# Kernel optimization log

Measured on AMD Instinct MI355X. Metric: run time of the kernel, lower is better.

## Reference

```python
import jax, jax.numpy as jnp
import numpy as np

B, N, P_FEATS = 8, 4096, 3
WIDTH, HEADS, LAYERS, N_LAT = 768, 12, 8, 256
NUM_FREQS = 8
D_HEAD = WIDTH // HEADS
SCALE = 1.0 / np.sqrt(np.sqrt(D_HEAD))  # applied to q and k separately
IN_DIM = 3 * (1 + 2 * NUM_FREQS) + P_FEATS  # 54
EPS = 1e-5


def fourier_embed(pc):
    # pc: [B,N,3] -> [B,N,51] (include_input + sin/cos at freqs 2^0..2^7)
    freqs = (2.0 ** jnp.arange(NUM_FREQS)).astype(pc.dtype)
    ang = pc[..., None] * freqs  # [B,N,3,F]
    ang = ang.reshape(*pc.shape[:-1], 3 * NUM_FREQS)
    return jnp.concatenate([pc, jnp.sin(ang), jnp.cos(ang)], axis=-1)


def layernorm(x, s, b):
    mu = jnp.mean(x, axis=-1, keepdims=True)
    var = jnp.mean(jnp.square(x - mu), axis=-1, keepdims=True)
    return (x - mu) * jax.lax.rsqrt(var + EPS) * s + b


def mh_attn(q, k, v):
    # q: [B,T,H,C], k/v: [B,S,H,C]
    w = jnp.einsum('bthc,bshc->bhts', q * SCALE, k * SCALE)
    w = jax.nn.softmax(w.astype(jnp.float32), axis=-1).astype(q.dtype)
    out = jnp.einsum('bhts,bshc->bthc', w, v)
    return out.reshape(*q.shape[:2], -1)


def setup_inputs() -> dict:
    key = jax.random.key(0)
    ks = iter(jax.random.split(key, 64))
    rn = lambda shape, std=0.02: jax.random.normal(next(ks), shape, jnp.float32) * std
    inp = {
        'pc': jax.random.normal(next(ks), (B, N, 3), jnp.float32),
        'feats': jax.random.uniform(next(ks), (B, N, P_FEATS), jnp.float32),
        'query': rn((N_LAT, WIDTH)),
        'in_W': rn((WIDTH, IN_DIM)), 'in_b': jnp.zeros((WIDTH,)),
        'ca_qkv_W': rn((3 * WIDTH, WIDTH)), 'ca_qkv_b': jnp.zeros((3 * WIDTH,)),
        'ca_proj_W': rn((WIDTH, WIDTH)), 'ca_proj_b': jnp.zeros((WIDTH,)),
        'ln1_s': jnp.ones((LAYERS, WIDTH)), 'ln1_b': jnp.zeros((LAYERS, WIDTH)),
        'qkv_W': rn((LAYERS, 3 * WIDTH, WIDTH)), 'qkv_b': jnp.zeros((LAYERS, 3 * WIDTH)),
        'proj_W': rn((LAYERS, WIDTH, WIDTH)), 'proj_b': jnp.zeros((LAYERS, WIDTH)),
        'ln2_s': jnp.ones((LAYERS, WIDTH)), 'ln2_b': jnp.zeros((LAYERS, WIDTH)),
        'fc_W': rn((LAYERS, 4 * WIDTH, WIDTH)), 'fc_b': jnp.zeros((LAYERS, 4 * WIDTH)),
        'fc2_W': rn((LAYERS, WIDTH, 4 * WIDTH)), 'fc2_b': jnp.zeros((LAYERS, WIDTH)),
    }
    return inp


def _forward(pc, feats, query, in_W, in_b, ca_qkv_W, ca_qkv_b, ca_proj_W, ca_proj_b,
             ln1_s, ln1_b, qkv_W, qkv_b, proj_W, proj_b, ln2_s, ln2_b,
             fc_W, fc_b, fc2_W, fc2_b):
    bs = pc.shape[0]
    data = jnp.concatenate([fourier_embed(pc), feats], axis=-1)  # [B,N,54]
    data = data @ in_W.T + in_b  # [B,N,W]
    q_lat = jnp.broadcast_to(query[None], (bs, N_LAT, WIDTH))

    # --- cross attention (no residual, matching source) ---
    q = (q_lat @ ca_qkv_W.T + ca_qkv_b)[..., :WIDTH]
    kv = data @ ca_qkv_W.T + ca_qkv_b
    k, v = kv[..., WIDTH:2 * WIDTH], kv[..., 2 * WIDTH:]
    q = q.reshape(bs, N_LAT, HEADS, D_HEAD)
    k = k.reshape(bs, N, HEADS, D_HEAD)
    v = v.reshape(bs, N, HEADS, D_HEAD)
    latents = mh_attn(q, k, v) @ ca_proj_W.T + ca_proj_b  # [B,L,W]

    # --- self-attention transformer stack via scan ---
    def block(x, p):
        (l1s, l1b, qW, qb, pW, pb, l2s, l2b, fW, fb, f2W, f2b) = p
        h = layernorm(x, l1s, l1b)
        qkv = (h @ qW.T + qb).reshape(bs, N_LAT, HEADS, 3 * D_HEAD)
        qh, kh, vh = jnp.split(qkv, 3, axis=-1)
        x = x + mh_attn(qh, kh, vh) @ pW.T + pb
        h = layernorm(x, l2s, l2b)
        h = jax.nn.gelu(h @ fW.T + fb, approximate=False) @ f2W.T + f2b
        return x + h, None

    params = (ln1_s, ln1_b, qkv_W, qkv_b, proj_W, proj_b, ln2_s, ln2_b, fc_W, fc_b, fc2_W, fc2_b)
    latents, _ = jax.lax.scan(block, latents, params)
    return latents, pc


def reference(pc, feats, query, in_W, in_b, ca_qkv_W, ca_qkv_b, ca_proj_W, ca_proj_b,
              ln1_s, ln1_b, qkv_W, qkv_b, proj_W, proj_b, ln2_s, ln2_b,
              fc_W, fc_b, fc2_W, fc2_b):
    return _forward(pc, feats, query, in_W, in_b, ca_qkv_W, ca_qkv_b, ca_proj_W, ca_proj_b,
                    ln1_s, ln1_b, qkv_W, qkv_b, proj_W, proj_b, ln2_s, ln2_b,
                    fc_W, fc_b, fc2_W, fc2_b)
```

## Files before the change

kernel.cpp:

```cpp
#include <hip/hip_runtime.h>
#include <stdint.h>

typedef unsigned short u16;
typedef __bf16 bf16x8 __attribute__((ext_vector_type(8)));
typedef float f32x4 __attribute__((ext_vector_type(4)));

#define DEVINL __device__ __forceinline__

DEVINL u16 f2bf(float f) {
  union { float f; unsigned u; } c; c.f = f;
  unsigned u = c.u + 0x7FFFu + ((c.u >> 16) & 1u);
  return (u16)(u >> 16);
}

DEVINL float bf2f(u16 v) {
  union { unsigned u; float f; } c; c.u = (unsigned)v << 16;
  return c.f;
}

DEVINL unsigned pk2bf(float a, float b) {
#if __has_builtin(__builtin_amdgcn_cvt_pk_bf16_f32)
  auto r = __builtin_amdgcn_cvt_pk_bf16_f32(a, b);
  unsigned u;
  __builtin_memcpy(&u, &r, 4);
  return u;
#else
  return (unsigned)f2bf(a) | ((unsigned)f2bf(b) << 16);
#endif
}

DEVINL void gl2lds16(const void* g, void* l) {
  __builtin_amdgcn_global_load_lds(
      (const __attribute__((address_space(1))) unsigned int*)g,
      (__attribute__((address_space(3))) unsigned int*)l, 16, 0, 0);
}

__global__ __launch_bounds__(256) void cvt4_kernel(
    const float* __restrict__ s0, u16* __restrict__ d0, int n0,
    const float* __restrict__ s1, u16* __restrict__ d1, int n1,
    const float* __restrict__ s2, u16* __restrict__ d2, int n2,
    const float* __restrict__ s3, u16* __restrict__ d3, int n3) {
  int i = blockIdx.x * 256 + threadIdx.x;
  const float* s; u16* d;
  if (i < n0) { s = s0; d = d0; }
  else {
    i -= n0;
    if (i < n1) { s = s1; d = d1; }
    else {
      i -= n1;
      if (i < n2) { s = s2; d = d2; }
      else {
        i -= n2;
        if (i >= n3) return;
        s = s3; d = d3;
      }
    }
  }
  float4 v = ((const float4*)s)[i];
  ((uint2*)d)[i] = make_uint2(pk2bf(v.x, v.y), pk2bf(v.z, v.w));
}

__global__ __launch_bounds__(256) void pad_inwT_kernel(const float* __restrict__ src,
                                                       u16* __restrict__ dst) {
  int t = blockIdx.x * 256 + threadIdx.x;
  if (t >= 64 * 768) return;
  int j = t / 768, o = t - j * 768;
  dst[t] = (j < 54) ? f2bf(src[o * 54 + j]) : (u16)0;
}

__global__ __launch_bounds__(256) void bprime_kernel(const float* __restrict__ caW,
                                                     const float* __restrict__ caB,
                                                     const float* __restrict__ inb,
                                                     float* __restrict__ bp) {
  int w = threadIdx.x >> 6, lane = threadIdx.x & 63;
  int m = blockIdx.x * 4 + w;
  const float* row = caW + (size_t)(768 + m) * 768;
  float s = 0.f;
#pragma unroll
  for (int k = 0; k < 12; k++) s += row[lane + k * 64] * inb[lane + k * 64];
#pragma unroll
  for (int msk = 32; msk >= 1; msk >>= 1) s += __shfl_xor(s, msk, 64);
  if (lane == 0) bp[m] = s + caB[768 + m];
}

__global__ __launch_bounds__(256) void embed_kernel(const float* __restrict__ pc,
                                                    const float* __restrict__ feats,
                                                    u16* __restrict__ emb) {
  int t = blockIdx.x * 256 + threadIdx.x;
  int p = t >> 6, c = t & 63;
  float v = 0.f;
  if (c < 3) {
    v = pc[p * 3 + c];
  } else if (c < 27) {
    int i = c - 3;
    float f = (float)(1 << (i & 7));
    v = sinf(pc[p * 3 + (i >> 3)] * f);
  } else if (c < 51) {
    int i = c - 27;
    float f = (float)(1 << (i & 7));
    v = cosf(pc[p * 3 + (i >> 3)] * f);
  } else if (c < 54) {
    v = feats[p * 3 + (c - 51)];
  }
  emb[t] = f2bf(v);
}

template <int TM, int TN, int WR, int WC, int MODE>
__global__ __launch_bounds__(256) void gemm_t(
    const u16* __restrict__ A, const u16* __restrict__ Bw,
    const float* __restrict__ bias, const float* __restrict__ resid,
    float* __restrict__ outF, u16* __restrict__ outB,
    int M, int N, int Nout, int K, int gelu,
    u16* __restrict__ vt, int vy, int skvt, int bsh) {
  constexpr int IM = TM / WR / 16;
  constexpr int IN = TN / WC / 16;
  __shared__ u16 As[TM * 32];
  __shared__ u16 Bs[TN * 32];
  const int tid = threadIdx.x;
  const int lane = tid & 63, w = tid >> 6;
  const int l15 = lane & 15, quad = lane >> 4;
  const int mblk = blockIdx.x * TM, nblk = blockIdx.y * TN;
  const int wm = (w % WR) * (TM / WR);
  const int wn = (w / WR) * (TN / WC);

  f32x4 acc[IM][IN];
#pragma unroll
  for (int i = 0; i < IM; i++)
#pragma unroll
    for (int j = 0; j < IN; j++) acc[i][j] = f32x4{0.f, 0.f, 0.f, 0.f};

  bool tv = false;
  if (MODE == 1) tv = ((int)blockIdx.y >= vy);
  if (MODE == 2) tv = ((int)(blockIdx.y % 3) == 2);

  if (!tv) {
    for (int k0 = 0; k0 < K; k0 += 32) {
#pragma unroll
      for (int s = tid; s < TM * 4; s += 256) {
        int row = s >> 2, c8 = (s & 3) << 3;
        gl2lds16(A + (size_t)(mblk + row) * K + (k0 + c8), &As[s * 8]);
      }
#pragma unroll
      for (int s = tid; s < TN * 4; s += 256) {
        int row = s >> 2, c8 = (s & 3) << 3;
        gl2lds16(Bw + (size_t)(nblk + row) * K + (k0 + c8), &Bs[s * 8]);
      }
      __syncthreads();
      bf16x8 af[IM], bfr[IN];
#pragma unroll
      for (int i = 0; i < IM; i++)
        af[i] = *(const bf16x8*)&As[(wm + i * 16 + l15) * 32 + quad * 8];
#pragma unroll
      for (int j = 0; j < IN; j++)
        bfr[j] = *(const bf16x8*)&Bs[(wn + j * 16 + l15) * 32 + quad * 8];
#pragma unroll
      for (int i = 0; i < IM; i++)
#pragma unroll
        for (int j = 0; j < IN; j++)
          acc[i][j] = __builtin_amdgcn_mfma_f32_16x16x32_bf16(bfr[j], af[i], acc[i][j], 0, 0, 0);
      __syncthreads();
    }
#pragma unroll
    for (int i = 0; i < IM; i++) {
      int m = mblk + wm + i * 16 + l15;
#pragma unroll
      for (int j = 0; j < IN; j++) {
        int n0 = nblk + wn + j * 16 + quad * 4;
        float4 bv = bias ? *(const float4*)&bias[n0] : make_float4(0.f, 0.f, 0.f, 0.f);
        float v0 = acc[i][j][0] + bv.x;
        float v1 = acc[i][j][1] + bv.y;
        float v2 = acc[i][j][2] + bv.z;
        float v3 = acc[i][j][3] + bv.w;
        if (gelu) {
          v0 = 0.5f * v0 * (1.0f + erff(v0 * 0.70710678118f));
          v1 = 0.5f * v1 * (1.0f + erff(v1 * 0.70710678118f));
          v2 = 0.5f * v2 * (1.0f + erff(v2 * 0.70710678118f));
          v3 = 0.5f * v3 * (1.0f + erff(v3 * 0.70710678118f));
        }
        size_t idx = (size_t)m * Nout + n0;
        if (resid) {
          float4 rv = *(const float4*)&resid[idx];
          v0 += rv.x; v1 += rv.y; v2 += rv.z; v3 += rv.w;
        }
        if (outF) {
          float4 ov = {v0, v1, v2, v3};
          *(float4*)&outF[idx] = ov;
        }
        if (outB) {
          *(uint2*)&outB[idx] = make_uint2(pk2bf(v0, v1), pk2bf(v2, v3));
        }
      }
    }
  } else {
    for (int k0 = 0; k0 < K; k0 += 32) {
#pragma unroll
      for (int s = tid; s < TM * 4; s += 256) {
        int row = s >> 2, c8 = (s & 3) << 3;
        gl2lds16(A + (size_t)(mblk + row) * K + (k0 + c8), &As[s * 8]);
      }
#pragma unroll
      for (int s = tid; s < TN * 4; s += 256) {
        int row = s >> 2, c8 = (s & 3) << 3;
        gl2lds16(Bw + (size_t)(nblk + row) * K + (k0 + c8), &Bs[s * 8]);
      }
      __syncthreads();
      bf16x8 af[IM], bfr[IN];
#pragma unroll
      for (int i = 0; i < IM; i++)
        af[i] = *(const bf16x8*)&As[(wm + i * 16 + l15) * 32 + quad * 8];
#pragma unroll
      for (int j = 0; j < IN; j++)
        bfr[j] = *(const bf16x8*)&Bs[(wn + j * 16 + l15) * 32 + quad * 8];
#pragma unroll
      for (int i = 0; i < IM; i++)
#pragma unroll
        for (int j = 0; j < IN; j++)
          acc[i][j] = __builtin_amdgcn_mfma_f32_16x16x32_bf16(af[i], bfr[j], acc[i][j], 0, 0, 0);
      __syncthreads();
    }
    int msk = (1 << bsh) - 1;
#pragma unroll
    for (int j = 0; j < IN; j++) {
      int n = nblk + wn + j * 16 + l15;
      float bv = bias ? bias[n] : 0.f;
#pragma unroll
      for (int i = 0; i < IM; i++) {
        int m0 = mblk + wm + i * 16 + quad * 4;
        int b = m0 >> bsh;
        int s0 = m0 & msk;
        float v0 = acc[i][j][0] + bv;
        float v1 = acc[i][j][1] + bv;
        float v2 = acc[i][j][2] + bv;
        float v3 = acc[i][j][3] + bv;
        size_t vrow;
        if (MODE == 2) {
          int h = blockIdx.y / 3;
          vrow = (size_t)(b * 12 + h) * 64 + (wn + j * 16 + l15);
        } else {
          vrow = (size_t)b * 768 + (n - vy * TN);
        }
        size_t addr = vrow * skvt + s0;
        *(uint2*)&vt[addr] = make_uint2(pk2bf(v0, v1), pk2bf(v2, v3));
      }
    }
  }
}

__global__ __launch_bounds__(256) void flash_kernel(
    const u16* __restrict__ Q, long qb, int qrs, int qhs,
    const u16* __restrict__ Kp, long kb, int krs, int khs,
    const u16* __restrict__ Vt, u16* __restrict__ Out,
    u16* __restrict__ Part, float* __restrict__ Ml,
    int Skv, int nsplit, int kvlen, int nbh, float scale2) {
  __shared__ u16 Qs[64 * 64];
  __shared__ u16 Ks[64 * 64];
  __shared__ u16 Vs[64 * 64];
  __shared__ u16 Ps[64 * 72];

  const int tid = threadIdx.x;
  const int lane = tid & 63, w = tid >> 6;
  const int l15 = lane & 15, quad = lane >> 4;

  int bid = blockIdx.x;
  int grp = nbh * nsplit;
  int qt = bid / grp;
  int rem = bid - qt * grp;
  int bh = rem / nsplit;
  int split = rem - bh * nsplit;
  int h = bh % 12, b = bh / 12;

  const u16* Qbase = Q + (size_t)b * qb + (size_t)(qt * 64) * qrs + h * qhs;
  const u16* Kbase = Kp + (size_t)b * kb + (size_t)h * khs;
  const u16* Vbase = Vt + ((size_t)(b * 12 + h) * 64) * Skv;

#pragma unroll
  for (int p = 0; p < 2; ++p) {
    int slot = tid + p * 256;
    int row = slot >> 3, c = slot & 7;
    int cg = (c - row) & 7;
    gl2lds16(Qbase + (size_t)row * qrs + cg * 8, &Qs[slot * 8]);
  }
  __syncthreads();

  bf16x8 qa[2];
#pragma unroll
  for (int kk = 0; kk < 2; kk++)
    qa[kk] = *(const bf16x8*)&Qs[(w * 16 + l15) * 64 + ((kk * 4 + quad + l15) & 7) * 8];

  f32x4 zero = {0.f, 0.f, 0.f, 0.f};
  f32x4 O[4];
#pragma unroll
  for (int d = 0; d < 4; d++) O[d] = zero;
  float m_i = -1e30f, l_i = 0.f;

  int kt0 = split * kvlen;
  for (int kt = kt0; kt < kt0 + kvlen; kt += 64) {
#pragma unroll
    for (int p = 0; p < 2; ++p) {
      int slot = tid + p * 256;
      int row = slot >> 3, c = slot & 7;
      int cg = (c - row) & 7;
      gl2lds16(Kbase + (size_t)(kt + row) * krs + cg * 8, &Ks[slot * 8]);
      gl2lds16(Vbase + (size_t)row * Skv + kt + cg * 8, &Vs[slot * 8]);
    }
    __syncthreads();

    f32x4 St[4];
#pragma unroll
    for (int j = 0; j < 4; j++) St[j] = zero;
#pragma unroll
    for (int kk = 0; kk < 2; kk++) {
#pragma unroll
      for (int j = 0; j < 4; j++) {
        bf16x8 kf = *(const bf16x8*)&Ks[(j * 16 + l15) * 64 + ((kk * 4 + quad + l15) & 7) * 8];
        St[j] = __builtin_amdgcn_mfma_f32_16x16x32_bf16(kf, qa[kk], St[j], 0, 0, 0);
      }
    }

    float mx = St[0][0];
#pragma unroll
    for (int j = 0; j < 4; j++)
#pragma unroll
      for (int r = 0; r < 4; r++) mx = fmaxf(mx, St[j][r]);
    mx = fmaxf(mx, __shfl_xor(mx, 16, 64));
    mx = fmaxf(mx, __shfl_xor(mx, 32, 64));
    mx *= scale2;
    float mnew = fmaxf(m_i, mx);
    float al = __expf(m_i - mnew);
    m_i = mnew;
    float sum = 0.f;
#pragma unroll
    for (int j = 0; j < 4; j++) {
      float p0 = __expf(fmaf(St[j][0], scale2, -mnew));
      float p1 = __expf(fmaf(St[j][1], scale2, -mnew));
      float p2 = __expf(fmaf(St[j][2], scale2, -mnew));
      float p3 = __expf(fmaf(St[j][3], scale2, -mnew));
      sum += (p0 + p1) + (p2 + p3);
      *(uint2*)&Ps[(w * 16 + l15) * 72 + j * 16 + quad * 4] =
          make_uint2(pk2bf(p0, p1), pk2bf(p2, p3));
    }
    sum += __shfl_xor(sum, 16, 64);
    sum += __shfl_xor(sum, 32, 64);
    l_i = l_i * al + sum;

    float a0 = __shfl(al, quad * 20 + 0, 64);
    float a1 = __shfl(al, quad * 20 + 1, 64);
    float a2 = __shfl(al, quad * 20 + 2, 64);
    float a3 = __shfl(al, quad * 20 + 3, 64);
#pragma unroll
    for (int d = 0; d < 4; d++) {
      O[d][0] *= a0; O[d][1] *= a1; O[d][2] *= a2; O[d][3] *= a3;
    }
    __asm__ __volatile__("s_waitcnt lgkmcnt(0)" ::: "memory");
#pragma unroll
    for (int kk = 0; kk < 2; kk++) {
      bf16x8 pa = *(const bf16x8*)&Ps[(w * 16 + l15) * 72 + kk * 32 + quad * 8];
#pragma unroll
      for (int d = 0; d < 4; d++) {
        bf16x8 vf = *(const bf16x8*)&Vs[(d * 16 + l15) * 64 + ((kk * 4 + quad + l15) & 7) * 8];
        O[d] = __builtin_amdgcn_mfma_f32_16x16x32_bf16(pa, vf, O[d], 0, 0, 0);
      }
    }
    __syncthreads();
  }

  float l0 = __shfl(l_i, quad * 20 + 0, 64);
  float l1 = __shfl(l_i, quad * 20 + 1, 64);
  float l2 = __shfl(l_i, quad * 20 + 2, 64);
  float l3 = __shfl(l_i, quad * 20 + 3, 64);

  if (nsplit == 1) {
    float inv0 = 1.f / l0, inv1 = 1.f / l1, inv2 = 1.f / l2, inv3 = 1.f / l3;
    u16* Ob = Out + ((size_t)(b * 256 + qt * 64 + w * 16 + quad * 4)) * 768 + h * 64 + l15;
#pragma unroll
    for (int d = 0; d < 4; d++) {
      Ob[(size_t)0 * 768 + d * 16] = f2bf(O[d][0] * inv0);
      Ob[(size_t)1 * 768 + d * 16] = f2bf(O[d][1] * inv1);
      Ob[(size_t)2 * 768 + d * 16] = f2bf(O[d][2] * inv2);
      Ob[(size_t)3 * 768 + d * 16] = f2bf(O[d][3] * inv3);
    }
  } else {
    float m0 = __shfl(m_i, quad * 20 + 0, 64);
    float m1 = __shfl(m_i, quad * 20 + 1, 64);
    float m2 = __shfl(m_i, quad * 20 + 2, 64);
    float m3 = __shfl(m_i, quad * 20 + 3, 64);
    u16* Pb = Part + ((size_t)(bh * 4 + qt) * nsplit + split) * 4096;
    int rowb = w * 16 + quad * 4;
#pragma unroll
    for (int d = 0; d < 4; d++) {
      Pb[(rowb + 0) * 64 + d * 16 + l15] = f2bf(O[d][0]);
      Pb[(rowb + 1) * 64 + d * 16 + l15] = f2bf(O[d][1]);
      Pb[(rowb + 2) * 64 + d * 16 + l15] = f2bf(O[d][2]);
      Pb[(rowb + 3) * 64 + d * 16 + l15] = f2bf(O[d][3]);
    }
    if (l15 == 0) {
      float* MlB = Ml + ((size_t)(bh * 4 + qt) * nsplit + split) * 128;
      MlB[rowb + 0] = m0; MlB[rowb + 1] = m1; MlB[rowb + 2] = m2; MlB[rowb + 3] = m3;
      MlB[64 + rowb + 0] = l0; MlB[64 + rowb + 1] = l1;
      MlB[64 + rowb + 2] = l2; MlB[64 + rowb + 3] = l3;
    }
  }
}

__global__ __launch_bounds__(256) void freduce_kernel(
    const u16* __restrict__ Part, const float* __restrict__ Ml,
    u16* __restrict__ Out, int nsplit) {
  int bid = blockIdx.x;
  int qt = bid & 3, bh = bid >> 2;
  int h = bh % 12, b = bh / 12;
  int tid = threadIdx.x;
  int r = tid >> 2, dc = tid & 3;
  const float* mlb = Ml + (size_t)(bh * 4 + qt) * nsplit * 128;
  float M = -1e30f;
  for (int s = 0; s < nsplit; s++) M = fmaxf(M, mlb[s * 128 + r]);
  float L = 0.f;
  float accv[16];
#pragma unroll
  for (int i = 0; i < 16; i++) accv[i] = 0.f;
  const u16* pb = Part + (size_t)(bh * 4 + qt) * nsplit * 4096 + r * 64 + dc * 16;
  for (int s = 0; s < nsplit; s++) {
    float wgt = __expf(mlb[s * 128 + r] - M);
    L += wgt * mlb[s * 128 + 64 + r];
    u16 tmp[16];
    *(uint4*)tmp = *(const uint4*)(pb + s * 4096);
    *(uint4*)(tmp + 8) = *(const uint4*)(pb + s * 4096 + 8);
#pragma unroll
    for (int i = 0; i < 16; i++) accv[i] += wgt * bf2f(tmp[i]);
  }
  float inv = 1.f / L;
  unsigned ot[8];
#pragma unroll
  for (int i = 0; i < 8; i++)
    ot[i] = pk2bf(accv[2 * i] * inv, accv[2 * i + 1] * inv);
  u16* ob = Out + ((size_t)(b * 256 + qt * 64 + r)) * 768 + h * 64 + dc * 16;
  *(uint4*)ob = *(uint4*)ot;
  *(uint4*)(ob + 8) = *(uint4*)(ot + 4);
}

__global__ __launch_bounds__(256) void ln_kernel(const float* __restrict__ X,
                                                 const float* __restrict__ sc,
                                                 const float* __restrict__ bi,
                                                 u16* __restrict__ Hout) {
  int row = blockIdx.x;
  int tid = threadIdx.x;
  const float* x = X + (size_t)row * 768;
  float v0 = x[tid], v1 = x[tid + 256], v2 = x[tid + 512];
  float s = v0 + v1 + v2;
  float q = v0 * v0 + v1 * v1 + v2 * v2;
#pragma unroll
  for (int m = 1; m < 64; m <<= 1) {
    s += __shfl_xor(s, m, 64);
    q += __shfl_xor(q, m, 64);
  }
  __shared__ float rs[4], rq[4];
  if ((tid & 63) == 0) { rs[tid >> 6] = s; rq[tid >> 6] = q; }
  __syncthreads();
  s = rs[0] + rs[1] + rs[2] + rs[3];
  q = rq[0] + rq[1] + rq[2] + rq[3];
  float mu = s * (1.f / 768.f);
  float var = q * (1.f / 768.f) - mu * mu;
  float rstd = rsqrtf(var + 1e-5f);
  u16* ho = Hout + (size_t)row * 768;
  ho[tid]       = f2bf((v0 - mu) * rstd * sc[tid]       + bi[tid]);
  ho[tid + 256] = f2bf((v1 - mu) * rstd * sc[tid + 256] + bi[tid + 256]);
  ho[tid + 512] = f2bf((v2 - mu) * rstd * sc[tid + 512] + bi[tid + 512]);
}

__global__ __launch_bounds__(256) void copy4_kernel(const float* __restrict__ src,
                                                    float* __restrict__ dst, int n4) {
  int i = blockIdx.x * 256 + threadIdx.x;
  if (i < n4) ((float4*)dst)[i] = ((const float4*)src)[i];
}

extern "C" void kernel_launch(void* const* d_in, const int* in_sizes, int n_in,
                              void* d_out, int out_size, void* d_ws, size_t ws_size,
                              hipStream_t stream) {
  const float* pc        = (const float*)d_in[0];
  const float* feats     = (const float*)d_in[1];
  const float* query     = (const float*)d_in[2];
  const float* in_W      = (const float*)d_in[3];
  const float* in_b      = (const float*)d_in[4];
  const float* ca_qkv_W  = (const float*)d_in[5];
  const float* ca_qkv_b  = (const float*)d_in[6];
  const float* ca_proj_W = (const float*)d_in[7];
  const float* ca_proj_b = (const float*)d_in[8];
  const float* ln1_s     = (const float*)d_in[9];
  const float* ln1_b     = (const float*)d_in[10];
  const float* qkv_W     = (const float*)d_in[11];
  const float* qkv_b     = (const float*)d_in[12];
  const float* proj_W    = (const float*)d_in[13];
  const float* proj_b    = (const float*)d_in[14];
  const float* ln2_s     = (const float*)d_in[15];
  const float* ln2_b     = (const float*)d_in[16];
  const float* fc_W      = (const float*)d_in[17];
  const float* fc_b      = (const float*)d_in[18];
  const float* fc2_W     = (const float*)d_in[19];
  const float* fc2_b     = (const float*)d_in[20];

  char* base = (char*)d_ws;
  size_t off = 0;
  auto alloc = [&](size_t bytes) -> char* {
    char* p = base + off;
    off += (bytes + 255) & ~(size_t)255;
    return p;
  };

  u16* WqT     = (u16*)alloc(64 * 768 * 2);
  u16* Wquery  = (u16*)alloc(256 * 768 * 2);
  u16* Wcaqkv  = (u16*)alloc(2304 * 768 * 2);
  u16* Wcaproj = (u16*)alloc(768 * 768 * 2);
  u16* Wkp     = (u16*)alloc(1536 * 64 * 2);
  float* bprime = (float*)alloc(1536 * 4);
  u16* qc      = (u16*)alloc(256 * 768 * 2);
  u16* attn    = (u16*)alloc((size_t)2048 * 768 * 2);
  u16* hbuf    = (u16*)alloc((size_t)2048 * 768 * 2);
  char* uni    = alloc(13369344);
  u16* qkvb    = (u16*)uni;
  u16* VtS     = (u16*)(uni + 9437184);
  u16* fc1     = (u16*)uni;
  u16* Part    = (u16*)uni;
  float* Ml    = (float*)(uni + 12582912);

  size_t fixed_end = off;
  const size_t wAllSz = (size_t)8 * (2304 * 768 + 768 * 768 + 2 * 3072 * 768) * 2;
  auto crossSz = [](int cb) {
    return (size_t)cb * 4096 * 64 * 2 + 2 * ((size_t)cb * 4096 * 768 * 2);
  };

  bool allw; int CB;
  if (fixed_end + (wAllSz > crossSz(8) ? wAllSz : crossSz(8)) + 65536 <= ws_size) {
    allw = true;  CB = 8;
  } else if (fixed_end + 14155776 + crossSz(2) + 65536 <= ws_size) {
    allw = false; CB = 2;
  } else {
    allw = false; CB = 1;
  }

  u16 *WqkvB, *WprojB, *WfcB, *Wfc2B, *emb, *kvbK, *VtC;
  if (allw) {
    char* X = base + off;
    WqkvB  = (u16*)X;
    WprojB = WqkvB + (size_t)8 * 2304 * 768;
    WfcB   = WprojB + (size_t)8 * 768 * 768;
    Wfc2B  = WfcB + (size_t)8 * 3072 * 768;
    emb  = (u16*)X;
    kvbK = (u16*)(X + (size_t)CB * 4096 * 64 * 2);
    VtC  = (u16*)(X + (size_t)CB * 4096 * 64 * 2 + (size_t)CB * 4096 * 768 * 2);
  } else {
    WqkvB  = (u16*)alloc(2304 * 768 * 2);
    WprojB = (u16*)alloc(768 * 768 * 2);
    WfcB   = (u16*)alloc(3072 * 768 * 2);
    Wfc2B  = (u16*)alloc((size_t)768 * 3072 * 2);
    emb  = (u16*)alloc((size_t)CB * 4096 * 64 * 2);
    kvbK = (u16*)alloc((size_t)CB * 4096 * 768 * 2);
    VtC  = (u16*)alloc((size_t)CB * 4096 * 768 * 2);
  }

  float* latents = (float*)d_out;
  const float scale2 = 0.125f;

  {
    int n0 = 256 * 768 / 4, n1 = 2304 * 768 / 4, n2 = 768 * 768 / 4;
    cvt4_kernel<<<(n0 + n1 + n2 + 255) / 256, 256, 0, stream>>>(
        query, Wquery, n0, ca_qkv_W, Wcaqkv, n1, ca_proj_W, Wcaproj, n2,
        nullptr, nullptr, 0);
  }
  pad_inwT_kernel<<<192, 256, 0, stream>>>(in_W, WqT);
  gemm_t<64, 64, 2, 2, 0><<<dim3(24, 1), 256, 0, stream>>>(
      Wcaqkv + (size_t)768 * 768, WqT, nullptr, nullptr, nullptr, Wkp,
      1536, 64, 64, 768, 0, nullptr, 0, 0, 0);
  bprime_kernel<<<384, 256, 0, stream>>>(ca_qkv_W, ca_qkv_b, in_b, bprime);

  gemm_t<64, 64, 2, 2, 0><<<dim3(4, 12), 256, 0, stream>>>(
      Wquery, Wcaqkv, ca_qkv_b, nullptr, nullptr, qc,
      256, 768, 768, 768, 0, nullptr, 0, 0, 0);

  int nchunk = 8 / CB;
  for (int c = 0; c < nchunk; ++c) {
    int Mc = CB * 4096;
    const float* pc_c = pc + (size_t)c * Mc * 3;
    const float* ft_c = feats + (size_t)c * Mc * 3;
    embed_kernel<<<Mc / 4, 256, 0, stream>>>(pc_c, ft_c, emb);
    gemm_t<128, 128, 2, 2, 1><<<dim3(Mc / 128, 12), 256, 0, stream>>>(
        emb, Wkp, bprime, nullptr, nullptr, kvbK,
        Mc, 1536, 768, 64, 0, VtC, 6, 4096, 12);
    flash_kernel<<<CB * 12 * 16, 256, 0, stream>>>(
        qc, 0L, 768, 64, kvbK, (long)4096 * 768, 768, 64, VtC,
        nullptr, Part, Ml, 4096, 4, 1024, CB * 12, scale2);
    freduce_kernel<<<CB * 48, 256, 0, stream>>>(
        Part, Ml, attn + (size_t)c * CB * 256 * 768, 4);
  }
  gemm_t<64, 64, 2, 2, 0><<<dim3(32, 12), 256, 0, stream>>>(
      attn, Wcaproj, ca_proj_b, nullptr, latents, nullptr,
      2048, 768, 768, 768, 0, nullptr, 0, 0, 0);

  if (allw) {
    int n0 = 8 * 2304 * 768 / 4, n1 = 8 * 768 * 768 / 4, n2 = 8 * 3072 * 768 / 4;
    cvt4_kernel<<<(n0 + n1 + 2 * n2 + 255) / 256, 256, 0, stream>>>(
        qkv_W, WqkvB, n0, proj_W, WprojB, n1, fc_W, WfcB, n2, fc2_W, Wfc2B, n2);
  }

  for (int l = 0; l < 8; ++l) {
    u16* Wlq  = allw ? WqkvB  + (size_t)l * 2304 * 768 : WqkvB;
    u16* Wlp  = allw ? WprojB + (size_t)l * 768 * 768  : WprojB;
    u16* Wlf  = allw ? WfcB   + (size_t)l * 3072 * 768 : WfcB;
    u16* Wlf2 = allw ? Wfc2B  + (size_t)l * 3072 * 768 : Wfc2B;
    if (!allw) {
      int n0 = 2304 * 768 / 4, n1 = 768 * 768 / 4, n2 = 3072 * 768 / 4;
      cvt4_kernel<<<(n0 + n1 + 2 * n2 + 255) / 256, 256, 0, stream>>>(
          qkv_W + (size_t)l * 2304 * 768, Wlq, n0,
          proj_W + (size_t)l * 768 * 768, Wlp, n1,
          fc_W + (size_t)l * 3072 * 768, Wlf, n2,
          fc2_W + (size_t)l * 768 * 3072, Wlf2, n2);
    }
    ln_kernel<<<2048, 256, 0, stream>>>(latents, ln1_s + l * 768, ln1_b + l * 768, hbuf);
    gemm_t<64, 64, 2, 2, 2><<<dim3(32, 36), 256, 0, stream>>>(
        hbuf, Wlq, qkv_b + l * 2304, nullptr, nullptr, qkvb,
        2048, 2304, 2304, 768, 0, VtS, 0, 256, 8);
    flash_kernel<<<384, 256, 0, stream>>>(
        qkvb, (long)256 * 2304, 2304, 192, qkvb + 64, (long)256 * 2304, 2304, 192,
        VtS, attn, nullptr, nullptr, 256, 1, 256, 96, scale2);
    gemm_t<64, 64, 2, 2, 0><<<dim3(32, 12), 256, 0, stream>>>(
        attn, Wlp, proj_b + l * 768, latents, latents, nullptr,
        2048, 768, 768, 768, 0, nullptr, 0, 0, 0);
    ln_kernel<<<2048, 256, 0, stream>>>(latents, ln2_s + l * 768, ln2_b + l * 768, hbuf);
    gemm_t<64, 128, 1, 4, 0><<<dim3(32, 24), 256, 0, stream>>>(
        hbuf, Wlf, fc_b + l * 3072, nullptr, nullptr, fc1,
        2048, 3072, 3072, 768, 1, nullptr, 0, 0, 0);
    gemm_t<64, 64, 2, 2, 0><<<dim3(32, 12), 256, 0, stream>>>(
        fc1, Wlf2, fc2_b + l * 768, latents, latents, nullptr,
        2048, 768, 768, 3072, 0, nullptr, 0, 0, 0);
  }

  copy4_kernel<<<96, 256, 0, stream>>>(pc, (float*)d_out + (size_t)2048 * 768, 98304 / 4);
}
```

Baseline: 1.333 ms.

## Double-buffer LDS tiles in GEMM and flash attention kernels

Both the GEMM kernel and the flash attention kernel now keep two LDS buffers for the A/B (or K/V) tiles. The first tile is loaded before the loop, and each iteration issues the global-to-LDS copy for the next K step into the other buffer before computing on the current one. This drops one barrier per iteration and is meant to overlap global memory latency with MFMA work. In exchange, LDS use per block roughly doubles for the staged tiles, which can lower occupancy. The overlap also depends on the barrier waiting for the async copies to complete.

```diff
diff --git a/kernel.cpp b/kernel.cpp
--- a/kernel.cpp
+++ b/kernel.cpp
@@ -114,8 +114,8 @@
     u16* __restrict__ vt, int vy, int skvt, int bsh) {
   constexpr int IM = TM / WR / 16;
   constexpr int IN = TN / WC / 16;
-  __shared__ u16 As[TM * 32];
-  __shared__ u16 Bs[TN * 32];
+  __shared__ u16 As[2][TM * 32];
+  __shared__ u16 Bs[2][TN * 32];
   const int tid = threadIdx.x;
   const int lane = tid & 63, w = tid >> 6;
   const int l15 = lane & 15, quad = lane >> 4;
@@ -133,32 +133,39 @@
   if (MODE == 1) tv = ((int)blockIdx.y >= vy);
   if (MODE == 2) tv = ((int)(blockIdx.y % 3) == 2);
 
+  auto stage = [&](int bi, int k0) {
+#pragma unroll
+    for (int s = tid; s < TM * 4; s += 256) {
+      int row = s >> 2, c8 = (s & 3) << 3;
+      gl2lds16(A + (size_t)(mblk + row) * K + (k0 + c8), &As[bi][s * 8]);
+    }
+#pragma unroll
+    for (int s = tid; s < TN * 4; s += 256) {
+      int row = s >> 2, c8 = (s & 3) << 3;
+      gl2lds16(Bw + (size_t)(nblk + row) * K + (k0 + c8), &Bs[bi][s * 8]);
+    }
+  };
+
   if (!tv) {
+    stage(0, 0);
+    __syncthreads();
+    int cur = 0;
     for (int k0 = 0; k0 < K; k0 += 32) {
-#pragma unroll
-      for (int s = tid; s < TM * 4; s += 256) {
-        int row = s >> 2, c8 = (s & 3) << 3;
-        gl2lds16(A + (size_t)(mblk + row) * K + (k0 + c8), &As[s * 8]);
-      }
-#pragma unroll
-      for (int s = tid; s < TN * 4; s += 256) {
-        int row = s >> 2, c8 = (s & 3) << 3;
-        gl2lds16(Bw + (size_t)(nblk + row) * K + (k0 + c8), &Bs[s * 8]);
-      }
-      __syncthreads();
+      if (k0 + 32 < K) stage(cur ^ 1, k0 + 32);
       bf16x8 af[IM], bfr[IN];
 #pragma unroll
       for (int i = 0; i < IM; i++)
-        af[i] = *(const bf16x8*)&As[(wm + i * 16 + l15) * 32 + quad * 8];
+        af[i] = *(const bf16x8*)&As[cur][(wm + i * 16 + l15) * 32 + quad * 8];
 #pragma unroll
       for (int j = 0; j < IN; j++)
-        bfr[j] = *(const bf16x8*)&Bs[(wn + j * 16 + l15) * 32 + quad * 8];
+        bfr[j] = *(const bf16x8*)&Bs[cur][(wn + j * 16 + l15) * 32 + quad * 8];
 #pragma unroll
       for (int i = 0; i < IM; i++)
 #pragma unroll
         for (int j = 0; j < IN; j++)
           acc[i][j] = __builtin_amdgcn_mfma_f32_16x16x32_bf16(bfr[j], af[i], acc[i][j], 0, 0, 0);
       __syncthreads();
+      cur ^= 1;
     }
 #pragma unroll
     for (int i = 0; i < IM; i++) {
@@ -192,31 +199,25 @@
       }
     }
   } else {
+    stage(0, 0);
+    __syncthreads();
+    int cur = 0;
     for (int k0 = 0; k0 < K; k0 += 32) {
-#pragma unroll
-      for (int s = tid; s < TM * 4; s += 256) {
-        int row = s >> 2, c8 = (s & 3) << 3;
-        gl2lds16(A + (size_t)(mblk + row) * K + (k0 + c8), &As[s * 8]);
-      }
-#pragma unroll
-      for (int s = tid; s < TN * 4; s += 256) {
-        int row = s >> 2, c8 = (s & 3) << 3;
-        gl2lds16(Bw + (size_t)(nblk + row) * K + (k0 + c8), &Bs[s * 8]);
-      }
-      __syncthreads();
+      if (k0 + 32 < K) stage(cur ^ 1, k0 + 32);
       bf16x8 af[IM], bfr[IN];
 #pragma unroll
       for (int i = 0; i < IM; i++)
-        af[i] = *(const bf16x8*)&As[(wm + i * 16 + l15) * 32 + quad * 8];
+        af[i] = *(const bf16x8*)&As[cur][(wm + i * 16 + l15) * 32 + quad * 8];
 #pragma unroll
       for (int j = 0; j < IN; j++)
-        bfr[j] = *(const bf16x8*)&Bs[(wn + j * 16 + l15) * 32 + quad * 8];
+        bfr[j] = *(const bf16x8*)&Bs[cur][(wn + j * 16 + l15) * 32 + quad * 8];
 #pragma unroll
       for (int i = 0; i < IM; i++)
 #pragma unroll
         for (int j = 0; j < IN; j++)
           acc[i][j] = __builtin_amdgcn_mfma_f32_16x16x32_bf16(af[i], bfr[j], acc[i][j], 0, 0, 0);
       __syncthreads();
+      cur ^= 1;
     }
     int msk = (1 << bsh) - 1;
 #pragma unroll
@@ -253,8 +254,8 @@
     u16* __restrict__ Part, float* __restrict__ Ml,
     int Skv, int nsplit, int kvlen, int nbh, float scale2) {
   __shared__ u16 Qs[64 * 64];
-  __shared__ u16 Ks[64 * 64];
-  __shared__ u16 Vs[64 * 64];
+  __shared__ u16 Ks[2][64 * 64];
+  __shared__ u16 Vs[2][64 * 64];
   __shared__ u16 Ps[64 * 72];
 
   const int tid = threadIdx.x;
@@ -273,12 +274,16 @@
   const u16* Kbase = Kp + (size_t)b * kb + (size_t)h * khs;
   const u16* Vbase = Vt + ((size_t)(b * 12 + h) * 64) * Skv;
 
+  int kt0 = split * kvlen;
+
 #pragma unroll
   for (int p = 0; p < 2; ++p) {
     int slot = tid + p * 256;
     int row = slot >> 3, c = slot & 7;
     int cg = (c - row) & 7;
     gl2lds16(Qbase + (size_t)row * qrs + cg * 8, &Qs[slot * 8]);
+    gl2lds16(Kbase + (size_t)(kt0 + row) * krs + cg * 8, &Ks[0][slot * 8]);
+    gl2lds16(Vbase + (size_t)row * Skv + kt0 + cg * 8, &Vs[0][slot * 8]);
   }
   __syncthreads();
 
@@ -293,17 +298,18 @@
   for (int d = 0; d < 4; d++) O[d] = zero;
   float m_i = -1e30f, l_i = 0.f;
 
-  int kt0 = split * kvlen;
+  int cur = 0;
   for (int kt = kt0; kt < kt0 + kvlen; kt += 64) {
-#pragma unroll
-    for (int p = 0; p < 2; ++p) {
-      int slot = tid + p * 256;
-      int row = slot >> 3, c = slot & 7;
-      int cg = (c - row) & 7;
-      gl2lds16(Kbase + (size_t)(kt + row) * krs + cg * 8, &Ks[slot * 8]);
-      gl2lds16(Vbase + (size_t)row * Skv + kt + cg * 8, &Vs[slot * 8]);
-    }
-    __syncthreads();
+    if (kt + 64 < kt0 + kvlen) {
+#pragma unroll
+      for (int p = 0; p < 2; ++p) {
+        int slot = tid + p * 256;
+        int row = slot >> 3, c = slot & 7;
+        int cg = (c - row) & 7;
+        gl2lds16(Kbase + (size_t)(kt + 64 + row) * krs + cg * 8, &Ks[cur ^ 1][slot * 8]);
+        gl2lds16(Vbase + (size_t)row * Skv + (kt + 64) + cg * 8, &Vs[cur ^ 1][slot * 8]);
+      }
+    }
 
     f32x4 St[4];
 #pragma unroll
@@ -312,7 +318,7 @@
     for (int kk = 0; kk < 2; kk++) {
 #pragma unroll
       for (int j = 0; j < 4; j++) {
-        bf16x8 kf = *(const bf16x8*)&Ks[(j * 16 + l15) * 64 + ((kk * 4 + quad + l15) & 7) * 8];
+        bf16x8 kf = *(const bf16x8*)&Ks[cur][(j * 16 + l15) * 64 + ((kk * 4 + quad + l15) & 7) * 8];
         St[j] = __builtin_amdgcn_mfma_f32_16x16x32_bf16(kf, qa[kk], St[j], 0, 0, 0);
       }
     }
@@ -357,11 +363,12 @@
       bf16x8 pa = *(const bf16x8*)&Ps[(w * 16 + l15) * 72 + kk * 32 + quad * 8];
 #pragma unroll
       for (int d = 0; d < 4; d++) {
-        bf16x8 vf = *(const bf16x8*)&Vs[(d * 16 + l15) * 64 + ((kk * 4 + quad + l15) & 7) * 8];
+        bf16x8 vf = *(const bf16x8*)&Vs[cur][(d * 16 + l15) * 64 + ((kk * 4 + quad + l15) & 7) * 8];
         O[d] = __builtin_amdgcn_mfma_f32_16x16x32_bf16(pa, vf, O[d], 0, 0, 0);
       }
     }
     __syncthreads();
+    cur ^= 1;
   }
 
   float l0 = __shfl(l_i, quad * 20 + 0, 64);
```

New measurement: 1.333 ms. No clear change (+0.0%).
